# Optimization experiments

Hardware: AMD Instinct MI355X
Metric: run time of the kernel (lower is better)

Reference implementation:

```python
import jax, jax.numpy as jnp
import numpy as np

N = 150000        # active voxels
C = 64            # channels
G = 64            # n_groups (depthwise)
CI = C // G       # in channels per group = 1
CO = C // G       # out channels per group = 1
K = 27            # 3x3x3 kernel volume
BS = 2            # batch size
SS = (480, 360, 32)  # spatial shape (z, y, x)


def _build_pairs(rng):
    """Build submanifold conv indice pairs (gather/scatter maps) from real voxel geometry."""
    total = SS[0] * SS[1] * SS[2]
    per_b = N // BS
    idx_list = []
    for b in range(BS):
        flat = rng.choice(total, size=per_b, replace=False)
        z = flat // (SS[1] * SS[2])
        rem = flat % (SS[1] * SS[2])
        y = rem // SS[2]
        x = rem % SS[2]
        idx_list.append(np.stack([np.full(per_b, b), z, y, x], 1))
    indices = np.concatenate(idx_list).astype(np.int64)  # [N, 4] (b,z,y,x)
    mult = np.array([total, SS[1] * SS[2], SS[2], 1], dtype=np.int64)
    keys = indices @ mult
    order = np.argsort(keys)
    sk = keys[order]
    offsets = np.array([(dz, dy, dx) for dz in (-1, 0, 1) for dy in (-1, 0, 1) for dx in (-1, 0, 1)], dtype=np.int64)
    pair_in = np.zeros((K, N), np.int64)
    pair_out = np.zeros((K, N), np.int64)
    mask = np.zeros((K, N), np.bool_)
    ar = np.arange(N, dtype=np.int64)
    for k in range(K):
        nb = indices.copy()
        nb[:, 1:] += offsets[k]
        inb = ((nb[:, 1] >= 0) & (nb[:, 1] < SS[0]) &
               (nb[:, 2] >= 0) & (nb[:, 2] < SS[1]) &
               (nb[:, 3] >= 0) & (nb[:, 3] < SS[2]))
        nk = nb @ mult
        pos = np.clip(np.searchsorted(sk, nk), 0, N - 1)
        found = inb & (sk[pos] == nk)
        j = order[pos]
        pair_in[k] = np.where(found, j, 0)
        pair_out[k] = np.where(found, ar, 0)
        mask[k] = found
    return pair_in, pair_out, mask


def setup_inputs() -> dict:
    rng = np.random.default_rng(0)
    pair_in, pair_out, pair_mask = _build_pairs(rng)
    key = jax.random.key(0)
    kf, kw, kb = jax.random.split(key, 3)
    features = jax.random.normal(kf, (N, C), dtype=jnp.float32)
    weight = jax.random.normal(kw, (K, G, CI, CO), dtype=jnp.float32) * 0.1
    bias = jax.random.normal(kb, (G * CO,), dtype=jnp.float32)
    return {"features": features, "weight": weight, "bias": bias,
            "pair_in": jnp.asarray(pair_in), "pair_out": jnp.asarray(pair_out),
            "pair_mask": jnp.asarray(pair_mask)}


def reference(features, weight, bias, pair_in, pair_out, pair_mask):
    # Grouped submanifold sparse conv: gather -> grouped matmul -> scatter-add,
    # scanned over the K kernel offsets to keep peak memory at O(N*C).
    n = features.shape[0]
    f = features.reshape(n, G, CI)
    mask_f = pair_mask.astype(features.dtype)

    def body(out, kd):
        pin, pout, m, w = kd  # pin/pout: [N], m: [N], w: [G, CI, CO]
        g = f[pin] * m[:, None, None]                 # [N, G, CI] masked gather
        contrib = jnp.einsum('ngc,gco->ngo', g, w)    # grouped matmul
        return out.at[pout].add(contrib), None

    out0 = jnp.zeros((n, G, CO), features.dtype)
    out, _ = jax.lax.scan(body, out0, (pair_in, pair_out, mask_f, weight))
    return out.reshape(n, G * CO) + bias
```

## Files before the change

### kernel.cpp

```cpp
#include <hip/hip_runtime.h>


#define KVOL 27

typedef float vf4 __attribute__((ext_vector_type(4)));

__global__ __launch_bounds__(256) void spconv_meta_kernel(
    const int* __restrict__ pair_in,
    const int* __restrict__ pair_mask,
    unsigned int* __restrict__ bits_ws,
    int n)
{
    const int vox = blockIdx.x * 256 + threadIdx.x;
    if (vox >= n) return;

    unsigned int bits = 0;
    #pragma unroll
    for (int k = 0; k < KVOL; ++k) {
        const int mv = pair_mask[(size_t)k * n + vox];
        bits |= (mv != 0 ? 1u : 0u) << k;
    }
    const int pin13 = pair_in[(size_t)13 * n + vox];
    if ((bits & (1u << 13)) && pin13 == vox)
        bits = (bits & ~(1u << 13)) | 0x80000000u;

    bits_ws[vox] = bits;
}

#define GPW  2
#define VPB  32

__global__ __launch_bounds__(256) void spconv_dw_kernel(
    const float* __restrict__ features,
    const float* __restrict__ weight,
    const float* __restrict__ bias,
    const int* __restrict__ pair_in,
    const unsigned int* __restrict__ bits_ws,
    float* __restrict__ out,
    int n)
{
    const int t     = threadIdx.x;
    const int w     = t >> 6;
    const int lane  = t & 63;
    const int sub   = lane >> 4;
    const int c4    = lane & 15;
    const int wbase = blockIdx.x * VPB + w * (GPW * 4);

    int voxl[GPW], voxc[GPW];
    unsigned int bitsv[GPW];
    vf4 fc[GPW];
    #pragma unroll
    for (int g = 0; g < GPW; ++g) {
        voxl[g] = wbase + g * 4 + sub;
        voxc[g] = voxl[g] < n ? voxl[g] : (n - 1);
        bitsv[g] = bits_ws[voxc[g]];
        fc[g] = ((const vf4*)&features[(size_t)voxc[g] * 64])[c4];
    }

    const vf4 bv  = ((const vf4*)bias)[c4];
    const vf4 w13 = ((const vf4*)&weight[13 * 64])[c4];

    #pragma unroll
    for (int g = 0; g < GPW; ++g) {
        const unsigned int bits = bitsv[g];

        const float m13 = (bits & 0x80000000u) ? 1.0f : 0.0f;
        vf4 acc = bv + (fc[g] * m13) * w13;

        unsigned int res = bits & 0x07FFFFFFu;
        unsigned int uni = res | __shfl_xor(res, 16);
        uni |= __shfl_xor(uni, 32);
        uni = __builtin_amdgcn_readfirstlane(uni);

        while (uni) {
            const int k = __builtin_ctz(uni);
            uni &= uni - 1;
            const float sel = (res >> k) & 1u ? 1.0f : 0.0f;
            const int pin = pair_in[(size_t)k * n + voxc[g]];
            const vf4 f  = ((const vf4*)&features[(size_t)pin * 64])[c4];
            const vf4 wk = ((const vf4*)&weight[k * 64])[c4];
            acc += (f * sel) * wk;
        }

        if (voxl[g] < n)
            __builtin_nontemporal_store(acc,
                (vf4*)&out[(size_t)voxl[g] * 64 + c4 * 4]);
    }
}

extern "C" void kernel_launch(void* const* d_in, const int* in_sizes, int n_in,
                              void* d_out, int out_size, void* d_ws, size_t ws_size,
                              hipStream_t stream) {
    const float* features  = (const float*)d_in[0];
    const float* weight    = (const float*)d_in[1];
    const float* bias      = (const float*)d_in[2];
    const int* pair_in     = (const int*)d_in[3];
    const int* pair_mask   = (const int*)d_in[5];
    float* out             = (float*)d_out;
    unsigned int* bits_ws  = (unsigned int*)d_ws;

    const int n = in_sizes[0] / 64;

    const int blocks1 = (n + 255) / 256;
    spconv_meta_kernel<<<blocks1, 256, 0, stream>>>(pair_in, pair_mask, bits_ws, n);

    const int blocks2 = (n + VPB - 1) / VPB;
    spconv_dw_kernel<<<blocks2, 256, 0, stream>>>(
        features, weight, bias, pair_in, bits_ws, out, n);
}
```

Before: 132.8 us.

## Fuse mask-bit metadata kernel into depthwise conv kernel via shared memory

Merges the separate metadata kernel into the main conv kernel. Each block now builds its per-voxel neighbor bitmasks and pair_in indices in shared memory, using vectorized nontemporal mask loads and LDS atomicOr, then runs the gather loop from LDS. This removes one launch and the workspace round trip, and replaces the per-offset global pair_in loads in the inner loop with LDS reads. In exchange it adds block-level syncs and LDS atomics, and pair_in is only loaded where the mask is set.

```diff
diff --git a/kernel.cpp b/kernel.cpp
--- a/kernel.cpp
+++ b/kernel.cpp
@@ -2,67 +2,96 @@
 
 
 #define KVOL 27
+#define VPB  32
+#define GPW  2
 
 typedef float vf4 __attribute__((ext_vector_type(4)));
+typedef int   vi4 __attribute__((ext_vector_type(4)));
 
-__global__ __launch_bounds__(256) void spconv_meta_kernel(
-    const int* __restrict__ pair_in,
-    const int* __restrict__ pair_mask,
-    unsigned int* __restrict__ bits_ws,
-    int n)
-{
-    const int vox = blockIdx.x * 256 + threadIdx.x;
-    if (vox >= n) return;
-
-    unsigned int bits = 0;
-    #pragma unroll
-    for (int k = 0; k < KVOL; ++k) {
-        const int mv = pair_mask[(size_t)k * n + vox];
-        bits |= (mv != 0 ? 1u : 0u) << k;
-    }
-    const int pin13 = pair_in[(size_t)13 * n + vox];
-    if ((bits & (1u << 13)) && pin13 == vox)
-        bits = (bits & ~(1u << 13)) | 0x80000000u;
-
-    bits_ws[vox] = bits;
-}
-
-#define GPW  2
-#define VPB  32
-
-__global__ __launch_bounds__(256) void spconv_dw_kernel(
+__global__ __launch_bounds__(256) void spconv_fused_kernel(
     const float* __restrict__ features,
     const float* __restrict__ weight,
     const float* __restrict__ bias,
     const int* __restrict__ pair_in,
-    const unsigned int* __restrict__ bits_ws,
+    const int* __restrict__ pair_mask,
     float* __restrict__ out,
     int n)
 {
+    __shared__ unsigned int bits_s[VPB];
+    __shared__ int pins_s[KVOL * VPB];
+
     const int t     = threadIdx.x;
     const int w     = t >> 6;
     const int lane  = t & 63;
     const int sub   = lane >> 4;
     const int c4    = lane & 15;
-    const int wbase = blockIdx.x * VPB + w * (GPW * 4);
+    const int wbase = blockIdx.x * VPB;
 
-    int voxl[GPW], voxc[GPW];
-    unsigned int bitsv[GPW];
+    if (t < VPB) bits_s[t] = 0u;
+
+    int voxl[GPW];
     vf4 fc[GPW];
     #pragma unroll
     for (int g = 0; g < GPW; ++g) {
-        voxl[g] = wbase + g * 4 + sub;
-        voxc[g] = voxl[g] < n ? voxl[g] : (n - 1);
-        bitsv[g] = bits_ws[voxc[g]];
-        fc[g] = ((const vf4*)&features[(size_t)voxc[g] * 64])[c4];
+        voxl[g] = wbase + w * (GPW * 4) + g * 4 + sub;
+        const int voxc = voxl[g] < n ? voxl[g] : (n - 1);
+        fc[g] = ((const vf4*)&features[(size_t)voxc * 64])[c4];
     }
-
     const vf4 bv  = ((const vf4*)bias)[c4];
     const vf4 w13 = ((const vf4*)&weight[13 * 64])[c4];
 
+    __syncthreads();
+
+    if (((n & 3) == 0) && (wbase + VPB <= n)) {
+        const int e4 = t * 4;
+        if (e4 < KVOL * VPB) {
+            const int k  = e4 >> 5;
+            const int v0 = e4 & 31;
+            const vi4 m4 = __builtin_nontemporal_load(
+                (const vi4*)&pair_mask[(size_t)k * n + wbase + v0]);
+            #pragma unroll
+            for (int j = 0; j < 4; ++j) {
+                if (m4[j]) {
+                    const int v   = v0 + j;
+                    const int vox = wbase + v;
+                    const int pin = pair_in[(size_t)k * n + vox];
+                    if (k == 13 && pin == vox) {
+                        atomicOr(&bits_s[v], 0x80000000u);
+                    } else {
+                        pins_s[e4 + j] = pin;
+                        atomicOr(&bits_s[v], 1u << k);
+                    }
+                }
+            }
+        }
+    } else {
+        for (int r = 0; r < 4; ++r) {
+            const int e = r * 256 + t;
+            if (e < KVOL * VPB) {
+                const int k = e >> 5;
+                const int v = e & 31;
+                const int vox = wbase + v;
+                if (vox < n) {
+                    const int mv = pair_mask[(size_t)k * n + vox];
+                    if (mv) {
+                        const int pin = pair_in[(size_t)k * n + vox];
+                        if (k == 13 && pin == vox) {
+                            atomicOr(&bits_s[v], 0x80000000u);
+                        } else {
+                            pins_s[e] = pin;
+                            atomicOr(&bits_s[v], 1u << k);
+                        }
+                    }
+                }
+            }
+        }
+    }
+    __syncthreads();
+
     #pragma unroll
     for (int g = 0; g < GPW; ++g) {
-        const unsigned int bits = bitsv[g];
+        const int vloc = w * (GPW * 4) + g * 4 + sub;
+        const unsigned int bits = bits_s[vloc];
 
         const float m13 = (bits & 0x80000000u) ? 1.0f : 0.0f;
         vf4 acc = bv + (fc[g] * m13) * w13;
@@ -75,11 +104,11 @@
         while (uni) {
             const int k = __builtin_ctz(uni);
             uni &= uni - 1;
-            const float sel = (res >> k) & 1u ? 1.0f : 0.0f;
-            const int pin = pair_in[(size_t)k * n + voxc[g]];
+            const bool has = (res >> k) & 1u;
+            const int pin = has ? pins_s[k * VPB + vloc] : 0;
             const vf4 f  = ((const vf4*)&features[(size_t)pin * 64])[c4];
             const vf4 wk = ((const vf4*)&weight[k * 64])[c4];
-            acc += (f * sel) * wk;
+            acc += (f * (has ? 1.0f : 0.0f)) * wk;
         }
 
         if (voxl[g] < n)
@@ -97,14 +126,10 @@
     const int* pair_in     = (const int*)d_in[3];
     const int* pair_mask   = (const int*)d_in[5];
     float* out             = (float*)d_out;
-    unsigned int* bits_ws  = (unsigned int*)d_ws;
 
     const int n = in_sizes[0] / 64;
 
-    const int blocks1 = (n + 255) / 256;
-    spconv_meta_kernel<<<blocks1, 256, 0, stream>>>(pair_in, pair_mask, bits_ws, n);
-
-    const int blocks2 = (n + VPB - 1) / VPB;
-    spconv_dw_kernel<<<blocks2, 256, 0, stream>>>(
-        features, weight, bias, pair_in, bits_ws, out, n);
+    const int blocks = (n + VPB - 1) / VPB;
+    spconv_fused_kernel<<<blocks, 256, 0, stream>>>(
+        features, weight, bias, pair_in, pair_mask, out, n);
 }
```

New measurement: 130.3 us. About the same (-1.8%).
